# Optimization experiments

Hardware: AMD Instinct MI355X
Metric: run time of the kernel (lower is better)

## Reference

```python
import jax, jax.numpy as jnp
import numpy as np

NUM_USERS = 100000
NUM_ITEMS = 50000
EMB_DIM = 64
N_EDGES = 2000000
N_LAYERS = 3
N_NODES = NUM_USERS + NUM_ITEMS


def setup_inputs() -> dict:
    key = jax.random.key(0)
    k1, k2, k3, k4, k5 = jax.random.split(key, 5)
    user_emb = jax.random.normal(k1, (NUM_USERS, EMB_DIM), dtype=jnp.float32)
    item_emb = jax.random.normal(k2, (NUM_ITEMS, EMB_DIM), dtype=jnp.float32)
    edge_norm = jax.random.uniform(k3, (N_EDGES,), dtype=jnp.float32)
    edge_src = jax.random.randint(k4, (N_EDGES,), 0, N_NODES, dtype=jnp.int64) if jax.config.jax_enable_x64 else jax.random.randint(k4, (N_EDGES,), 0, N_NODES, dtype=jnp.int32)
    edge_dst = jax.random.randint(k5, (N_EDGES,), 0, N_NODES, dtype=edge_src.dtype)
    return {"user_emb": user_emb, "item_emb": item_emb, "edge_norm": edge_norm,
            "edge_src": edge_src, "edge_dst": edge_dst}


def reference(user_emb, item_emb, edge_norm, edge_src, edge_dst):
    # LightGCN propagation: ego[l+1][row] = sum_edges edge_norm * ego[l][col]
    ego = jnp.concatenate([user_emb, item_emb], axis=0)  # [N, D]
    acc = ego
    for _ in range(N_LAYERS):
        msg = ego[edge_dst] * edge_norm[:, None]          # [E, D] gather + scale
        ego = jax.ops.segment_sum(msg, edge_src, num_segments=N_NODES)  # scatter-add
        acc = acc + ego
    final = acc / (N_LAYERS + 1)
    return final[:NUM_USERS], final[NUM_USERS:]
```

## Files before the change

### kernel.cpp

```cpp
#include <hip/hip_runtime.h>
#include <hip/hip_fp16.h>


#define NUM_USERS 100000
#define NUM_ITEMS 50000
#define EMB_DIM   64
#define N_EDGES   2000000
#define N_NODES   (NUM_USERS + NUM_ITEMS)
#define NODE_FLOATS (N_NODES * EMB_DIM)
#define NODE_F4     (NODE_FLOATS / 4)

#define NBUCKET  512
#define NPB      293
#define NPART    8
#define NCNT     (NBUCKET * NPART)
#define BT       512
#define VPT      8
#define TILE     (BT * VPT)
#define NTILE    ((N_EDGES + TILE - 1) / TILE)

typedef unsigned int uint;
typedef unsigned short ushort;
typedef unsigned long long u64;

__device__ __forceinline__ float2 h2f2(uint u) {
    __half2 h = *reinterpret_cast<const __half2*>(&u);
    return __half22float2(h);
}
__device__ __forceinline__ uint f2h2(float a, float b) {
    __half2 h = __floats2half2_rn(a, b);
    return *reinterpret_cast<uint*>(&h);
}

__global__ void lgcn_init(const float4* __restrict__ user,
                          const float4* __restrict__ item,
                          uint2* __restrict__ egoA) {
    const int n_user4 = NUM_USERS * EMB_DIM / 4;
    for (int i = blockIdx.x * blockDim.x + threadIdx.x; i < NODE_F4;
         i += gridDim.x * blockDim.x) {
        float4 v = (i < n_user4) ? user[i] : item[i - n_user4];
        egoA[i] = make_uint2(f2h2(v.x, v.y), f2h2(v.z, v.w));
    }
}

__global__ void zero_ints(int* __restrict__ p, int n) {
    int i = blockIdx.x * blockDim.x + threadIdx.x;
    if (i < n) p[i] = 0;
}

__global__ __launch_bounds__(BT) void bucket_hist(const int* __restrict__ src,
                                                  int* __restrict__ bucketCount) {
    __shared__ int cnt[NBUCKET];
    int t = threadIdx.x;
    int part = blockIdx.x & (NPART - 1);
    cnt[t] = 0;
    __syncthreads();
    int base = blockIdx.x * TILE + t;
    #pragma unroll
    for (int k = 0; k < VPT; ++k) {
        int e = base + k * BT;
        if (e < N_EDGES) atomicAdd(&cnt[src[e] / NPB], 1);
    }
    __syncthreads();
    int c = cnt[t];
    if (c) atomicAdd(&bucketCount[t * NPART + part], c);
}

__global__ __launch_bounds__(1024) void bucket_scan(const int* __restrict__ bucketCount,
                                                    int* __restrict__ bucketOffset,
                                                    int* __restrict__ gCur,
                                                    int* __restrict__ rowPtr) {
    __shared__ int s[1024];
    int t = threadIdx.x;
    int4 c = *(const int4*)(bucketCount + t * 4);
    int sum = c.x + c.y + c.z + c.w;
    s[t] = sum;
    __syncthreads();
    for (int off = 1; off < 1024; off <<= 1) {
        int x = (t >= off) ? s[t - off] : 0;
        __syncthreads();
        s[t] += x;
        __syncthreads();
    }
    int base = s[t] - sum;
    int i0 = t * 4;
    bucketOffset[i0]     = base;
    bucketOffset[i0 + 1] = base + c.x;
    bucketOffset[i0 + 2] = base + c.x + c.y;
    bucketOffset[i0 + 3] = base + c.x + c.y + c.z;
    gCur[i0]     = base;
    gCur[i0 + 1] = base + c.x;
    gCur[i0 + 2] = base + c.x + c.y;
    gCur[i0 + 3] = base + c.x + c.y + c.z;
    if (t == 0) {
        bucketOffset[NCNT] = N_EDGES;
        rowPtr[N_NODES] = N_EDGES;
    }
}

__global__ __launch_bounds__(BT) void bucket_scatter(const int* __restrict__ src,
                                                     const int* __restrict__ dst,
                                                     const float* __restrict__ norm,
                                                     int* __restrict__ gCur,
                                                     u64* __restrict__ bpair) {
    __shared__ int cnt[NBUCKET];
    __shared__ int bbase[NBUCKET];
    int t = threadIdx.x;
    int part = blockIdx.x & (NPART - 1);
    cnt[t] = 0;
    __syncthreads();
    int base = blockIdx.x * TILE + t;
    #pragma unroll
    for (int k = 0; k < VPT; ++k) {
        int e = base + k * BT;
        if (e < N_EDGES) atomicAdd(&cnt[src[e] / NPB], 1);
    }
    __syncthreads();
    int c = cnt[t];
    bbase[t] = c ? atomicAdd(&gCur[t * NPART + part], c) : 0;
    __syncthreads();
    cnt[t] = 0;
    __syncthreads();
    #pragma unroll
    for (int k = 0; k < VPT; ++k) {
        int e = base + k * BT;
        if (e < N_EDGES) {
            int s = src[e];
            int b = s / NPB;
            int sl = s - b * NPB;
            int r = atomicAdd(&cnt[b], 1);
            uint lo = (uint)dst[e] | ((uint)sl << 18);
            u64 packed = (u64)lo | ((u64)(uint)__float_as_uint(norm[e]) << 32);
            bpair[bbase[b] + r] = packed;
        }
    }
}

__global__ __launch_bounds__(1024) void csr_finalize(const int* __restrict__ bucketOffset,
                                                     const u64* __restrict__ bpair,
                                                     int* __restrict__ rowPtr,
                                                     u64* __restrict__ pairs) {
    __shared__ int cnt[NBUCKET];
    __shared__ int cur[NBUCKET];
    int b = blockIdx.x;
    int t = threadIdx.x;
    int beg = bucketOffset[b * NPART];
    int end = bucketOffset[b * NPART + NPART];
    int nodeBase = b * NPB;

    if (t < NBUCKET) cnt[t] = 0;
    __syncthreads();
    for (int i = beg + t; i < end; i += 1024) {
        uint lo = (uint)bpair[i];
        atomicAdd(&cnt[(lo >> 18) & 0x1FF], 1);
    }
    __syncthreads();
    int v = (t < NBUCKET) ? cnt[t] : 0;
    for (int off = 1; off < NBUCKET; off <<= 1) {
        int x = (t >= off && t < NBUCKET) ? cnt[t - off] : 0;
        __syncthreads();
        if (t < NBUCKET) cnt[t] += x;
        __syncthreads();
    }
    if (t < NBUCKET) {
        int excl = cnt[t] - v;
        cur[t] = excl;
        int node = nodeBase + t;
        if (t < NPB && node < N_NODES) rowPtr[node] = beg + excl;
    }
    __syncthreads();
    for (int i = beg + t; i < end; i += 1024) {
        u64 p = bpair[i];
        int s = ((uint)p >> 18) & 0x1FF;
        int r = atomicAdd(&cur[s], 1);
        pairs[beg + r] = p;
    }
}

__global__ void lgcn_gather(const ushort* __restrict__ ego,
                            ushort* __restrict__ nego,
                            float* __restrict__ acc,
                            const ushort* __restrict__ e0,
                            const ushort* __restrict__ e1,
                            const int* __restrict__ rowPtr,
                            const u64* __restrict__ pairs,
                            int finalMode) {
    int node   = blockIdx.x * 8 + (threadIdx.x >> 5);
    int lane32 = threadIdx.x & 31;
    int g      = lane32 >> 3;
    int sub    = lane32 & 7;
    if (node >= N_NODES) return;
    int beg = rowPtr[node];
    int end = rowPtr[node + 1];

    float a0 = 0.f, a1 = 0.f, a2 = 0.f, a3 = 0.f;
    float a4 = 0.f, a5 = 0.f, a6 = 0.f, a7 = 0.f;
    float b0 = 0.f, b1 = 0.f, b2 = 0.f, b3 = 0.f;
    float b4 = 0.f, b5 = 0.f, b6 = 0.f, b7 = 0.f;

    int i = beg + g;
    for (; i + 4 < end; i += 8) {
        u64 pA = pairs[i];
        u64 pB = pairs[i + 4];
        uint loA = (uint)pA, loB = (uint)pB;
        float wA = __uint_as_float((uint)(pA >> 32));
        float wB = __uint_as_float((uint)(pB >> 32));
        uint4 rA = *(const uint4*)(ego + ((size_t)(loA & 0x3FFFF) << 6) + (sub << 3));
        uint4 rB = *(const uint4*)(ego + ((size_t)(loB & 0x3FFFF) << 6) + (sub << 3));
        float2 q;
        q = h2f2(rA.x); a0 += wA * q.x; a1 += wA * q.y;
        q = h2f2(rA.y); a2 += wA * q.x; a3 += wA * q.y;
        q = h2f2(rA.z); a4 += wA * q.x; a5 += wA * q.y;
        q = h2f2(rA.w); a6 += wA * q.x; a7 += wA * q.y;
        q = h2f2(rB.x); b0 += wB * q.x; b1 += wB * q.y;
        q = h2f2(rB.y); b2 += wB * q.x; b3 += wB * q.y;
        q = h2f2(rB.z); b4 += wB * q.x; b5 += wB * q.y;
        q = h2f2(rB.w); b6 += wB * q.x; b7 += wB * q.y;
    }
    if (i < end) {
        u64 p = pairs[i];
        uint lo = (uint)p;
        float w = __uint_as_float((uint)(p >> 32));
        uint4 r = *(const uint4*)(ego + ((size_t)(lo & 0x3FFFF) << 6) + (sub << 3));
        float2 q;
        q = h2f2(r.x); a0 += w * q.x; a1 += w * q.y;
        q = h2f2(r.y); a2 += w * q.x; a3 += w * q.y;
        q = h2f2(r.z); a4 += w * q.x; a5 += w * q.y;
        q = h2f2(r.w); a6 += w * q.x; a7 += w * q.y;
    }
    float s0 = a0 + b0, s1 = a1 + b1, s2 = a2 + b2, s3 = a3 + b3;
    float s4 = a4 + b4, s5 = a5 + b5, s6 = a6 + b6, s7 = a7 + b7;

    s0 += __shfl_down(s0, 16); s1 += __shfl_down(s1, 16);
    s2 += __shfl_down(s2, 16); s3 += __shfl_down(s3, 16);
    s4 += __shfl_down(s4, 16); s5 += __shfl_down(s5, 16);
    s6 += __shfl_down(s6, 16); s7 += __shfl_down(s7, 16);
    s0 += __shfl_down(s0, 8);  s1 += __shfl_down(s1, 8);
    s2 += __shfl_down(s2, 8);  s3 += __shfl_down(s3, 8);
    s4 += __shfl_down(s4, 8);  s5 += __shfl_down(s5, 8);
    s6 += __shfl_down(s6, 8);  s7 += __shfl_down(s7, 8);

    if (lane32 < 8) {
        size_t ro = ((size_t)node << 6) + (lane32 << 3);
        if (!finalMode) {
            uint4* np = (uint4*)(nego + ro);
            *np = make_uint4(f2h2(s0, s1), f2h2(s2, s3),
                             f2h2(s4, s5), f2h2(s6, s7));
        } else {
            uint4 z0 = *(const uint4*)(e0  + ro);
            uint4 z1 = *(const uint4*)(e1  + ro);
            uint4 z2 = *(const uint4*)(ego + ro);
            float2 a, b, c;
            float4 o0, o1;
            a = h2f2(z0.x); b = h2f2(z1.x); c = h2f2(z2.x);
            o0.x = (a.x + b.x + c.x + s0) * 0.25f;
            o0.y = (a.y + b.y + c.y + s1) * 0.25f;
            a = h2f2(z0.y); b = h2f2(z1.y); c = h2f2(z2.y);
            o0.z = (a.x + b.x + c.x + s2) * 0.25f;
            o0.w = (a.y + b.y + c.y + s3) * 0.25f;
            a = h2f2(z0.z); b = h2f2(z1.z); c = h2f2(z2.z);
            o1.x = (a.x + b.x + c.x + s4) * 0.25f;
            o1.y = (a.y + b.y + c.y + s5) * 0.25f;
            a = h2f2(z0.w); b = h2f2(z1.w); c = h2f2(z2.w);
            o1.z = (a.x + b.x + c.x + s6) * 0.25f;
            o1.w = (a.y + b.y + c.y + s7) * 0.25f;
            float4* ap = (float4*)(acc + ro);
            ap[0] = o0;
            ap[1] = o1;
        }
    }
}

extern "C" void kernel_launch(void* const* d_in, const int* in_sizes, int n_in,
                              void* d_out, int out_size, void* d_ws, size_t ws_size,
                              hipStream_t stream) {
    const float* user_emb  = (const float*)d_in[0];
    const float* item_emb  = (const float*)d_in[1];
    const float* edge_norm = (const float*)d_in[2];
    const int*   edge_src  = (const int*)d_in[3];
    const int*   edge_dst  = (const int*)d_in[4];
    float* acc = (float*)d_out;

    char* w = (char*)d_ws;
    ushort* egoA  = (ushort*)w;                      w += (size_t)NODE_FLOATS * 2;
    ushort* egoB  = (ushort*)w;                      w += (size_t)NODE_FLOATS * 2;
    u64*   pairs  = (u64*)w;                         w += (size_t)N_EDGES * 8;
    int*   rowPtr = (int*)w;                         w += (size_t)(N_NODES + 4) * 4;
    int*   bucketCount  = (int*)w;                   w += (size_t)NCNT * 4;
    int*   bucketOffset = (int*)w;                   w += (size_t)(NCNT + 4) * 4;
    int*   gCur   = (int*)w;                         w += (size_t)NCNT * 4;
    u64*   bpair  = (u64*)w;
    ushort* egoC  = (ushort*)w;

    const int T = 256;
    const int EW_BLOCKS = 2048;
    const int GATHER_BLOCKS = (N_NODES + 7) / 8;

    lgcn_init<<<EW_BLOCKS, T, 0, stream>>>(
        (const float4*)user_emb, (const float4*)item_emb, (uint2*)egoA);

    zero_ints<<<NCNT / T, T, 0, stream>>>(bucketCount, NCNT);
    bucket_hist<<<NTILE, BT, 0, stream>>>(edge_src, bucketCount);
    bucket_scan<<<1, 1024, 0, stream>>>(bucketCount, bucketOffset, gCur, rowPtr);
    bucket_scatter<<<NTILE, BT, 0, stream>>>(edge_src, edge_dst, edge_norm,
                                             gCur, bpair);
    csr_finalize<<<NBUCKET, 1024, 0, stream>>>(bucketOffset, bpair,
                                               rowPtr, pairs);

    lgcn_gather<<<GATHER_BLOCKS, T, 0, stream>>>(egoA, egoB, acc,
                                                 (const ushort*)0, (const ushort*)0,
                                                 rowPtr, pairs, 0);
    lgcn_gather<<<GATHER_BLOCKS, T, 0, stream>>>(egoB, egoC, acc,
                                                 (const ushort*)0, (const ushort*)0,
                                                 rowPtr, pairs, 0);
    lgcn_gather<<<GATHER_BLOCKS, T, 0, stream>>>(egoC, (ushort*)0, acc,
                                                 egoA, egoB,
                                                 rowPtr, pairs, 1);
}
```

Before: 334.4 us.

## Build CSR with per-node global atomic histogram and direct atomic scatter

Replaces the two-level bucketed CSR construction (bucket histogram, bucket scatter, per-bucket local sort) with a direct per-node histogram using global atomics, then a three-kernel hierarchical prefix scan, then an atomic-cursor scatter of packed (dst, norm) pairs straight into the final CSR array. This drops the intermediate bucket-pair buffer and one full pass over the edge payload. In exchange it relies on about four million random global atomics on a 150k-entry counter array. The edge order within each row becomes nondeterministic, so summation order can vary between runs. Node counter zeroing is folded into the init kernel.

```diff
diff --git a/kernel.cpp b/kernel.cpp
--- a/kernel.cpp
+++ b/kernel.cpp
@@ -10,14 +10,11 @@
 #define NODE_FLOATS (N_NODES * EMB_DIM)
 #define NODE_F4     (NODE_FLOATS / 4)
 
-#define NBUCKET  512
-#define NPB      293
-#define NPART    8
-#define NCNT     (NBUCKET * NPART)
-#define BT       512
-#define VPT      8
-#define TILE     (BT * VPT)
-#define NTILE    ((N_EDGES + TILE - 1) / TILE)
+#define NE4      (N_EDGES / 4)
+#define EHB      ((NE4 + 255) / 256)
+
+#define CHUNK    1024
+#define NCHUNK   ((N_NODES + CHUNK - 1) / CHUNK)
 
 typedef unsigned int uint;
 typedef unsigned short ushort;
@@ -34,147 +31,102 @@
 
 __global__ void lgcn_init(const float4* __restrict__ user,
                           const float4* __restrict__ item,
-                          uint2* __restrict__ egoA) {
+                          uint2* __restrict__ egoA,
+                          int* __restrict__ nodeCount) {
     const int n_user4 = NUM_USERS * EMB_DIM / 4;
-    for (int i = blockIdx.x * blockDim.x + threadIdx.x; i < NODE_F4;
-         i += gridDim.x * blockDim.x) {
+    int stride = gridDim.x * blockDim.x;
+    int gid = blockIdx.x * blockDim.x + threadIdx.x;
+    for (int i = gid; i < N_NODES; i += stride) nodeCount[i] = 0;
+    for (int i = gid; i < NODE_F4; i += stride) {
         float4 v = (i < n_user4) ? user[i] : item[i - n_user4];
         egoA[i] = make_uint2(f2h2(v.x, v.y), f2h2(v.z, v.w));
     }
 }
 
-__global__ void zero_ints(int* __restrict__ p, int n) {
+__global__ __launch_bounds__(256) void edge_hist(const int4* __restrict__ src4,
+                                                 int* __restrict__ nodeCount) {
     int i = blockIdx.x * blockDim.x + threadIdx.x;
-    if (i < n) p[i] = 0;
-}
-
-__global__ __launch_bounds__(BT) void bucket_hist(const int* __restrict__ src,
-                                                  int* __restrict__ bucketCount) {
-    __shared__ int cnt[NBUCKET];
+    if (i >= NE4) return;
+    int4 s = src4[i];
+    atomicAdd(&nodeCount[s.x], 1);
+    atomicAdd(&nodeCount[s.y], 1);
+    atomicAdd(&nodeCount[s.z], 1);
+    atomicAdd(&nodeCount[s.w], 1);
+}
+
+__global__ __launch_bounds__(CHUNK) void scanA(const int* __restrict__ nodeCount,
+                                               int* __restrict__ chunkSum) {
+    __shared__ int s[CHUNK];
     int t = threadIdx.x;
-    int part = blockIdx.x & (NPART - 1);
-    cnt[t] = 0;
+    int node = blockIdx.x * CHUNK + t;
+    s[t] = (node < N_NODES) ? nodeCount[node] : 0;
     __syncthreads();
-    int base = blockIdx.x * TILE + t;
-    #pragma unroll
-    for (int k = 0; k < VPT; ++k) {
-        int e = base + k * BT;
-        if (e < N_EDGES) atomicAdd(&cnt[src[e] / NPB], 1);
-    }
+    for (int off = CHUNK / 2; off > 0; off >>= 1) {
+        if (t < off) s[t] += s[t + off];
+        __syncthreads();
+    }
+    if (t == 0) chunkSum[blockIdx.x] = s[0];
+}
+
+__global__ __launch_bounds__(256) void scanB(const int* __restrict__ chunkSum,
+                                             int* __restrict__ chunkOff,
+                                             int* __restrict__ rowPtr) {
+    __shared__ int s[256];
+    int t = threadIdx.x;
+    int v = (t < NCHUNK) ? chunkSum[t] : 0;
+    s[t] = v;
     __syncthreads();
-    int c = cnt[t];
-    if (c) atomicAdd(&bucketCount[t * NPART + part], c);
-}
-
-__global__ __launch_bounds__(1024) void bucket_scan(const int* __restrict__ bucketCount,
-                                                    int* __restrict__ bucketOffset,
-                                                    int* __restrict__ gCur,
-                                                    int* __restrict__ rowPtr) {
-    __shared__ int s[1024];
+    for (int off = 1; off < 256; off <<= 1) {
+        int x = (t >= off) ? s[t - off] : 0;
+        __syncthreads();
+        s[t] += x;
+        __syncthreads();
+    }
+    if (t < NCHUNK) chunkOff[t] = s[t] - v;
+    if (t == 0) rowPtr[N_NODES] = N_EDGES;
+}
+
+__global__ __launch_bounds__(CHUNK) void scanC(const int* __restrict__ nodeCount,
+                                               const int* __restrict__ chunkOff,
+                                               int* __restrict__ rowPtr,
+                                               int* __restrict__ cur) {
+    __shared__ int s[CHUNK];
     int t = threadIdx.x;
-    int4 c = *(const int4*)(bucketCount + t * 4);
-    int sum = c.x + c.y + c.z + c.w;
-    s[t] = sum;
+    int node = blockIdx.x * CHUNK + t;
+    int v = (node < N_NODES) ? nodeCount[node] : 0;
+    s[t] = v;
     __syncthreads();
-    for (int off = 1; off < 1024; off <<= 1) {
+    for (int off = 1; off < CHUNK; off <<= 1) {
         int x = (t >= off) ? s[t - off] : 0;
         __syncthreads();
         s[t] += x;
         __syncthreads();
     }
-    int base = s[t] - sum;
-    int i0 = t * 4;
-    bucketOffset[i0]     = base;
-    bucketOffset[i0 + 1] = base + c.x;
-    bucketOffset[i0 + 2] = base + c.x + c.y;
-    bucketOffset[i0 + 3] = base + c.x + c.y + c.z;
-    gCur[i0]     = base;
-    gCur[i0 + 1] = base + c.x;
-    gCur[i0 + 2] = base + c.x + c.y;
-    gCur[i0 + 3] = base + c.x + c.y + c.z;
-    if (t == 0) {
-        bucketOffset[NCNT] = N_EDGES;
-        rowPtr[N_NODES] = N_EDGES;
-    }
-}
-
-__global__ __launch_bounds__(BT) void bucket_scatter(const int* __restrict__ src,
-                                                     const int* __restrict__ dst,
-                                                     const float* __restrict__ norm,
-                                                     int* __restrict__ gCur,
-                                                     u64* __restrict__ bpair) {
-    __shared__ int cnt[NBUCKET];
-    __shared__ int bbase[NBUCKET];
-    int t = threadIdx.x;
-    int part = blockIdx.x & (NPART - 1);
-    cnt[t] = 0;
-    __syncthreads();
-    int base = blockIdx.x * TILE + t;
-    #pragma unroll
-    for (int k = 0; k < VPT; ++k) {
-        int e = base + k * BT;
-        if (e < N_EDGES) atomicAdd(&cnt[src[e] / NPB], 1);
-    }
-    __syncthreads();
-    int c = cnt[t];
-    bbase[t] = c ? atomicAdd(&gCur[t * NPART + part], c) : 0;
-    __syncthreads();
-    cnt[t] = 0;
-    __syncthreads();
-    #pragma unroll
-    for (int k = 0; k < VPT; ++k) {
-        int e = base + k * BT;
-        if (e < N_EDGES) {
-            int s = src[e];
-            int b = s / NPB;
-            int sl = s - b * NPB;
-            int r = atomicAdd(&cnt[b], 1);
-            uint lo = (uint)dst[e] | ((uint)sl << 18);
-            u64 packed = (u64)lo | ((u64)(uint)__float_as_uint(norm[e]) << 32);
-            bpair[bbase[b] + r] = packed;
-        }
-    }
-}
-
-__global__ __launch_bounds__(1024) void csr_finalize(const int* __restrict__ bucketOffset,
-                                                     const u64* __restrict__ bpair,
-                                                     int* __restrict__ rowPtr,
-                                                     u64* __restrict__ pairs) {
-    __shared__ int cnt[NBUCKET];
-    __shared__ int cur[NBUCKET];
-    int b = blockIdx.x;
-    int t = threadIdx.x;
-    int beg = bucketOffset[b * NPART];
-    int end = bucketOffset[b * NPART + NPART];
-    int nodeBase = b * NPB;
-
-    if (t < NBUCKET) cnt[t] = 0;
-    __syncthreads();
-    for (int i = beg + t; i < end; i += 1024) {
-        uint lo = (uint)bpair[i];
-        atomicAdd(&cnt[(lo >> 18) & 0x1FF], 1);
-    }
-    __syncthreads();
-    int v = (t < NBUCKET) ? cnt[t] : 0;
-    for (int off = 1; off < NBUCKET; off <<= 1) {
-        int x = (t >= off && t < NBUCKET) ? cnt[t - off] : 0;
-        __syncthreads();
-        if (t < NBUCKET) cnt[t] += x;
-        __syncthreads();
-    }
-    if (t < NBUCKET) {
-        int excl = cnt[t] - v;
-        cur[t] = excl;
-        int node = nodeBase + t;
-        if (t < NPB && node < N_NODES) rowPtr[node] = beg + excl;
-    }
-    __syncthreads();
-    for (int i = beg + t; i < end; i += 1024) {
-        u64 p = bpair[i];
-        int s = ((uint)p >> 18) & 0x1FF;
-        int r = atomicAdd(&cur[s], 1);
-        pairs[beg + r] = p;
-    }
+    if (node < N_NODES) {
+        int val = chunkOff[blockIdx.x] + s[t] - v;
+        rowPtr[node] = val;
+        cur[node] = val;
+    }
+}
+
+__global__ __launch_bounds__(256) void edge_scatter(const int4* __restrict__ src4,
+                                                    const int4* __restrict__ dst4,
+                                                    const float4* __restrict__ norm4,
+                                                    int* __restrict__ cur,
+                                                    u64* __restrict__ pairs) {
+    int i = blockIdx.x * blockDim.x + threadIdx.x;
+    if (i >= NE4) return;
+    int4 s = src4[i];
+    int4 d = dst4[i];
+    float4 n = norm4[i];
+    int p0 = atomicAdd(&cur[s.x], 1);
+    pairs[p0] = (u64)(uint)d.x | ((u64)(uint)__float_as_uint(n.x) << 32);
+    int p1 = atomicAdd(&cur[s.y], 1);
+    pairs[p1] = (u64)(uint)d.y | ((u64)(uint)__float_as_uint(n.y) << 32);
+    int p2 = atomicAdd(&cur[s.z], 1);
+    pairs[p2] = (u64)(uint)d.z | ((u64)(uint)__float_as_uint(n.z) << 32);
+    int p3 = atomicAdd(&cur[s.w], 1);
+    pairs[p3] = (u64)(uint)d.w | ((u64)(uint)__float_as_uint(n.w) << 32);
 }
 
 __global__ void lgcn_gather(const ushort* __restrict__ ego,
@@ -286,26 +238,28 @@
     ushort* egoB  = (ushort*)w;                      w += (size_t)NODE_FLOATS * 2;
     u64*   pairs  = (u64*)w;                         w += (size_t)N_EDGES * 8;
     int*   rowPtr = (int*)w;                         w += (size_t)(N_NODES + 4) * 4;
-    int*   bucketCount  = (int*)w;                   w += (size_t)NCNT * 4;
-    int*   bucketOffset = (int*)w;                   w += (size_t)(NCNT + 4) * 4;
-    int*   gCur   = (int*)w;                         w += (size_t)NCNT * 4;
-    u64*   bpair  = (u64*)w;
-    ushort* egoC  = (ushort*)w;
+    ushort* egoC      = (ushort*)w;
+    int*   nodeCount  = (int*)w;                     w += (size_t)N_NODES * 4;
+    int*   cur        = (int*)w;                     w += (size_t)N_NODES * 4;
+    int*   chunkSum   = (int*)w;                     w += (size_t)(NCHUNK + 1) * 4;
+    int*   chunkOff   = (int*)w;
 
     const int T = 256;
     const int EW_BLOCKS = 2048;
     const int GATHER_BLOCKS = (N_NODES + 7) / 8;
 
     lgcn_init<<<EW_BLOCKS, T, 0, stream>>>(
-        (const float4*)user_emb, (const float4*)item_emb, (uint2*)egoA);
-
-    zero_ints<<<NCNT / T, T, 0, stream>>>(bucketCount, NCNT);
-    bucket_hist<<<NTILE, BT, 0, stream>>>(edge_src, bucketCount);
-    bucket_scan<<<1, 1024, 0, stream>>>(bucketCount, bucketOffset, gCur, rowPtr);
-    bucket_scatter<<<NTILE, BT, 0, stream>>>(edge_src, edge_dst, edge_norm,
-                                             gCur, bpair);
-    csr_finalize<<<NBUCKET, 1024, 0, stream>>>(bucketOffset, bpair,
-                                               rowPtr, pairs);
+        (const float4*)user_emb, (const float4*)item_emb, (uint2*)egoA,
+        nodeCount);
+
+    edge_hist<<<EHB, T, 0, stream>>>((const int4*)edge_src, nodeCount);
+    scanA<<<NCHUNK, CHUNK, 0, stream>>>(nodeCount, chunkSum);
+    scanB<<<1, 256, 0, stream>>>(chunkSum, chunkOff, rowPtr);
+    scanC<<<NCHUNK, CHUNK, 0, stream>>>(nodeCount, chunkOff, rowPtr, cur);
+    edge_scatter<<<EHB, T, 0, stream>>>((const int4*)edge_src,
+                                        (const int4*)edge_dst,
+                                        (const float4*)edge_norm,
+                                        cur, pairs);
 
     lgcn_gather<<<GATHER_BLOCKS, T, 0, stream>>>(egoA, egoB, acc,
                                                  (const ushort*)0, (const ushort*)0,
```

New measurement: 499.4 us. 49.3% more time.
